# Kernel tuning notes

Measured on AMD Instinct MI355X. Metric: run time of the kernel, lower is better.

Reference implementation:

```python
import jax, jax.numpy as jnp
import numpy as np

B, M, D, K = 512, 32, 2048, 3
COUPLING_STRENGTH = 0.1
SPATIAL_DECAY = 2.0


def setup_inputs() -> dict:
    key = jax.random.key(0)
    k1, k2 = jax.random.split(key)
    x = jax.random.normal(k1, (B, M, D), dtype=jnp.float32)  # stacked module activities
    w = jax.random.normal(k2, (D, K), dtype=jnp.float32) * 0.1  # conv1d weight [out=D, in=1, K] squeezed
    return {"x": x, "w": w}


def reference(x, w):
    # x: [B, M, D] stacked module activities; w: [D, K] field-propagation conv weight.
    b, m, d = x.shape
    k = w.shape[1]
    pad = k // 2
    # Conv1d(in=1, out=D, padding=pad) followed by mean over the length dim is
    # exactly: E[b,m,c] = (1/D) * sum_k w[c,k] * S_k, where S_k is the sum of x
    # over the input positions actually touched by tap k (zero padding drops edges).
    T = x.sum(-1)                       # [B, M] total sum
    cs = jnp.cumsum(x, axis=-1)         # [B, M, D] prefix sums
    S_list = []
    for kk in range(k):                 # K is a small static constant
        o = kk - pad                    # tap offset; touched indices [max(0,o), D-1+min(0,o)]
        if o > 0:
            S_list.append(T - cs[..., o - 1])       # drop first o entries
        elif o < 0:
            S_list.append(cs[..., d - 1 + o])       # drop last |o| entries
        else:
            S_list.append(T)
    S = jnp.stack(S_list, axis=-1)      # [B, M, K]
    fields = jnp.einsum('bmk,dk->bmd', S, w) / d  # electric fields [B, M, D]
    # distance-decayed coupling with self-term excluded (i != j in the loop)
    idx = jnp.arange(m)
    decay = jnp.exp(-jnp.abs(idx[:, None] - idx[None, :]).astype(x.dtype) / SPATIAL_DECAY)
    decay = decay * (1.0 - jnp.eye(m, dtype=x.dtype))  # zero diagonal
    weighted = jnp.einsum('ij,bjd->bid', decay, fields)  # [B, M, D]
    return x + COUPLING_STRENGTH * weighted
```

## Files before the change

### kernel.cpp

```cpp
#include <hip/hip_runtime.h>
#include <stdint.h>

#define B_ 512
#define M_ 32
#define D_ 2048
#define Q4 128

typedef float fvec4 __attribute__((ext_vector_type(4)));

static __device__ __forceinline__ uint32_t pk_bf16(float lo, float hi) {
    uint32_t r;
    asm("v_cvt_pk_bf16_f32 %0, %1, %2" : "=v"(r) : "v"(lo), "v"(hi));
    return r;
}
static __device__ __forceinline__ float bf_lo(uint32_t u) { return __uint_as_float(u << 16); }
static __device__ __forceinline__ float bf_hi(uint32_t u) { return __uint_as_float(u & 0xFFFF0000u); }

__global__ __launch_bounds__(1024, 4) void ephaptic_pipe(const float* __restrict__ x,
                                                         const float* __restrict__ w,
                                                         float* __restrict__ out) {
    const int tid = threadIdx.x;
    const int b0 = blockIdx.x * 2;

    __shared__ uint32_t sx[4][M_][256];
    __shared__ float sT[M_], sF[M_], sL[M_];
    __shared__ fvec4 sCA[M_], sCB[M_];

    const int m = tid >> 5;
    const int t = tid & 31;
    const int p4 = tid & 127;
    const int rg = tid >> 7;

    const fvec4* wf = (const fvec4*)w;

    float psum = 0.f, first = 0.f, last = 0.f;
    fvec4 v0, v1, v2, v3;

    auto RL = [&](int b, int rq) {
        const fvec4* row = (const fvec4*)(x + ((size_t)b * M_ + m) * (size_t)D_) + rq * Q4;
        v0 = row[t];  v1 = row[t + 32];  v2 = row[t + 64];  v3 = row[t + 96];
        asm volatile("" : "+v"(v0), "+v"(v1), "+v"(v2), "+v"(v3));
    };
    auto RS = [&](int rq) {
        psum += (v0.x+v0.y)+(v0.z+v0.w) + (v1.x+v1.y)+(v1.z+v1.w)
              + (v2.x+v2.y)+(v2.z+v2.w) + (v3.x+v3.y)+(v3.z+v3.w);
        if (rq == 0 && t == 0)  first = v0.x;
        if (rq == 3 && t == 31) last  = v3.w;
        uint2* sr = (uint2*)sx[rq][m];
        sr[t]      = make_uint2(pk_bf16(v0.x, v0.y), pk_bf16(v0.z, v0.w));
        sr[t + 32] = make_uint2(pk_bf16(v1.x, v1.y), pk_bf16(v1.z, v1.w));
        sr[t + 64] = make_uint2(pk_bf16(v2.x, v2.y), pk_bf16(v2.z, v2.w));
        sr[t + 96] = make_uint2(pk_bf16(v3.x, v3.y), pk_bf16(v3.z, v3.w));
    };
    auto SUMS = [&]() {
        float s = psum;
#pragma unroll
        for (int off = 16; off > 0; off >>= 1) s += __shfl_xor(s, off, 64);
        if (t == 0)  { sT[m] = s; sF[m] = first; }
        if (t == 31) { sL[m] = last; }
    };
    auto COEF = [&](fvec4* sC) {
        if (tid < M_) {
            const int i = tid;
            float r0 = 0.f, r1 = 0.f, r2 = 0.f;
            for (int j = 0; j < M_; ++j) {
                if (j == i) continue;
                const float dij = __expf(-0.5f * fabsf((float)(i - j)));
                const float T = sT[j];
                r0 += dij * (T - sL[j]);
                r1 += dij * T;
                r2 += dij * (T - sF[j]);
            }
            const float s = 0.1f / (float)D_;
            sC[i] = (fvec4){r0 * s, r1 * s, r2 * s, 0.f};
        }
    };
    auto W = [&](int b, int wq, const fvec4* sC) {
        const fvec4 w0 = wf[(wq * Q4 + p4) * 3 + 0];
        const fvec4 w1 = wf[(wq * Q4 + p4) * 3 + 1];
        const fvec4 w2 = wf[(wq * Q4 + p4) * 3 + 2];
        fvec4* ob = (fvec4*)(out + (size_t)b * M_ * D_) + wq * Q4 + p4;
#pragma unroll
        for (int rr = 0; rr < 4; ++rr) {
            const int r = rg * 4 + rr;
            const fvec4 c = sC[r];
            const uint2 u = ((const uint2*)sx[wq][r])[p4];
            fvec4 o;
            o.x = bf_lo(u.x) + c.x * w0.x + c.y * w0.y + c.z * w0.z;
            o.y = bf_hi(u.x) + c.x * w0.w + c.y * w1.x + c.z * w1.y;
            o.z = bf_lo(u.y) + c.x * w1.z + c.y * w1.w + c.z * w2.x;
            o.w = bf_hi(u.y) + c.x * w2.y + c.y * w2.z + c.z * w2.w;
            __builtin_nontemporal_store(o, ob + (size_t)r * 512);
        }
    };

    RL(b0, 0); RS(0);
    RL(b0, 1); RS(1);
    RL(b0, 2); RS(2);
    RL(b0, 3); RS(3);
    SUMS();
    __syncthreads();
    COEF(sCA);
    __syncthreads();
    W(b0, 0, sCA);
    __syncthreads();
    psum = 0.f;
    RL(b0 + 1, 0); W(b0, 1, sCA); RS(0);
    __syncthreads();
    RL(b0 + 1, 1); W(b0, 2, sCA); RS(1);
    __syncthreads();
    RL(b0 + 1, 2); W(b0, 3, sCA); RS(2);
    __syncthreads();
    RL(b0 + 1, 3); RS(3);
    SUMS();
    __syncthreads();
    COEF(sCB);
    __syncthreads();
    W(b0 + 1, 0, sCB);
    W(b0 + 1, 1, sCB);
    W(b0 + 1, 2, sCB);
    W(b0 + 1, 3, sCB);
}

extern "C" void kernel_launch(void* const* d_in, const int* in_sizes, int n_in,
                              void* d_out, int out_size, void* d_ws, size_t ws_size,
                              hipStream_t stream) {
    const float* x = (const float*)d_in[0];
    const float* w = (const float*)d_in[1];
    float* out = (float*)d_out;
    ephaptic_pipe<<<B_ / 2, 1024, 0, stream>>>(x, w, out);
}
```

Measured before the change: 51.96 us.

## Double-buffer global row loads in registers and use LDS-only barriers

New measurement: 47.26 us. 1.1x faster.

```diff
diff --git a/kernel.cpp b/kernel.cpp
--- a/kernel.cpp
+++ b/kernel.cpp
@@ -15,6 +15,11 @@
 }
 static __device__ __forceinline__ float bf_lo(uint32_t u) { return __uint_as_float(u << 16); }
 static __device__ __forceinline__ float bf_hi(uint32_t u) { return __uint_as_float(u & 0xFFFF0000u); }
+
+static __device__ __forceinline__ void lds_barrier() {
+    asm volatile("s_waitcnt lgkmcnt(0)" ::: "memory");
+    __builtin_amdgcn_s_barrier();
+}
 
 __global__ __launch_bounds__(1024, 4) void ephaptic_pipe(const float* __restrict__ x,
                                                          const float* __restrict__ w,
@@ -34,14 +39,14 @@
     const fvec4* wf = (const fvec4*)w;
 
     float psum = 0.f, first = 0.f, last = 0.f;
-    fvec4 v0, v1, v2, v3;
+    fvec4 a0, a1, a2, a3;
+    fvec4 e0, e1, e2, e3;
 
-    auto RL = [&](int b, int rq) {
+    auto RL = [&](int b, int rq, fvec4& v0, fvec4& v1, fvec4& v2, fvec4& v3) {
         const fvec4* row = (const fvec4*)(x + ((size_t)b * M_ + m) * (size_t)D_) + rq * Q4;
         v0 = row[t];  v1 = row[t + 32];  v2 = row[t + 64];  v3 = row[t + 96];
-        asm volatile("" : "+v"(v0), "+v"(v1), "+v"(v2), "+v"(v3));
     };
-    auto RS = [&](int rq) {
+    auto RS = [&](int rq, const fvec4& v0, const fvec4& v1, const fvec4& v2, const fvec4& v3) {
         psum += (v0.x+v0.y)+(v0.z+v0.w) + (v1.x+v1.y)+(v1.z+v1.w)
               + (v2.x+v2.y)+(v2.z+v2.w) + (v3.x+v3.y)+(v3.z+v3.w);
         if (rq == 0 && t == 0)  first = v0.x;
@@ -94,28 +99,29 @@
         }
     };
 
-    RL(b0, 0); RS(0);
-    RL(b0, 1); RS(1);
-    RL(b0, 2); RS(2);
-    RL(b0, 3); RS(3);
+    RL(b0, 0, a0, a1, a2, a3);
+    RL(b0, 1, e0, e1, e2, e3);
+    RS(0, a0, a1, a2, a3);  RL(b0, 2, a0, a1, a2, a3);
+    RS(1, e0, e1, e2, e3);  RL(b0, 3, e0, e1, e2, e3);
+    RS(2, a0, a1, a2, a3);
+    RS(3, e0, e1, e2, e3);
     SUMS();
-    __syncthreads();
+    lds_barrier();
     COEF(sCA);
-    __syncthreads();
-    W(b0, 0, sCA);
-    __syncthreads();
+    lds_barrier();
+
+    RL(b0 + 1, 0, a0, a1, a2, a3);  W(b0, 0, sCA);  lds_barrier();
+    RL(b0 + 1, 1, e0, e1, e2, e3);  W(b0, 1, sCA);  lds_barrier();
     psum = 0.f;
-    RL(b0 + 1, 0); W(b0, 1, sCA); RS(0);
-    __syncthreads();
-    RL(b0 + 1, 1); W(b0, 2, sCA); RS(1);
-    __syncthreads();
-    RL(b0 + 1, 2); W(b0, 3, sCA); RS(2);
-    __syncthreads();
-    RL(b0 + 1, 3); RS(3);
+    RS(0, a0, a1, a2, a3);  RL(b0 + 1, 2, a0, a1, a2, a3);  W(b0, 2, sCA);  lds_barrier();
+    RS(1, e0, e1, e2, e3);  RL(b0 + 1, 3, e0, e1, e2, e3);  W(b0, 3, sCA);  lds_barrier();
+    RS(2, a0, a1, a2, a3);
+    RS(3, e0, e1, e2, e3);
     SUMS();
-    __syncthreads();
+    lds_barrier();
     COEF(sCB);
-    __syncthreads();
+    lds_barrier();
+
     W(b0 + 1, 0, sCB);
     W(b0 + 1, 1, sCB);
     W(b0 + 1, 2, sCB);
```
